# Kernel optimization log

Measured on AMD Instinct MI355X. Metric: run time of the kernel, lower is better.

The kernel has to match this reference:

```python
import jax, jax.numpy as jnp
import numpy as np

B, S, H = 4, 4096, 1024
NUM_LEVELS, DECAY = 3, 0.8
D0, D1 = 512, 204  # int(1024*0.5), int(512*0.5*0.8)


def _xavier(key, shape):
    fan_in, fan_out = shape
    return jax.random.normal(key, shape, dtype=jnp.float32) * np.sqrt(2.0 / (fan_in + fan_out))


def setup_inputs() -> dict:
    key = jax.random.key(0)
    ks = jax.random.split(key, 8)
    return {
        "keys": jax.random.normal(ks[0], (B, S, H), dtype=jnp.float32),
        "values": jax.random.normal(ks[1], (B, S, H), dtype=jnp.float32),
        "importance": jax.random.uniform(ks[2], (B, S), dtype=jnp.float32),
        # encoder layers (stored as [in, out]; torch Linear applies x @ W.T + b)
        "We0": _xavier(ks[3], (H, D0)), "be0": jnp.zeros((D0,), jnp.float32),
        "We1": _xavier(ks[4], (D0, D1)), "be1": jnp.zeros((D1,), jnp.float32),
        # decoder layers
        "Wd0": _xavier(ks[5], (D0, H)), "bd0": jnp.zeros((H,), jnp.float32),
        "Wd1": _xavier(ks[6], (D1, D0)), "bd1": jnp.zeros((D0,), jnp.float32),
    }


def _level_sizes(n):
    sizes, remaining = [], n
    for i in range(NUM_LEVELS):
        if i == NUM_LEVELS - 1:
            sizes.append(remaining)
        else:
            sz = int(remaining * (1 - DECAY) * DECAY ** i)
            sizes.append(sz)
            remaining -= sz
    return sizes


def reference(keys, values, importance, We0, be0, We1, be1, Wd0, bd0, Wd1, bd1):
    n = B * S
    fk = keys.reshape(n, H)
    fv = values.reshape(n, H)
    sorted_idx = jnp.argsort(-importance.reshape(-1))  # descending importance
    sizes = _level_sizes(n)

    def chain(x, level):
        # encode 0..level-1 with ReLU, then decode level-1..0 with ReLU
        if level >= 1:
            x = jax.nn.relu(x @ We0 + be0)
        if level >= 2:
            x = jax.nn.relu(x @ We1 + be1)
            x = jax.nn.relu(x @ Wd1 + bd1)
        if level >= 1:
            x = jax.nn.relu(x @ Wd0 + bd0)
        return x

    ck = jnp.zeros_like(fk)
    cv = jnp.zeros_like(fv)
    start = 0
    for level, size in enumerate(sizes):
        if size <= 0:
            continue
        idx = jax.lax.dynamic_slice(sorted_idx, (start,), (size,))
        ck = ck.at[idx].set(chain(fk[idx], level))
        cv = cv.at[idx].set(chain(fv[idx], level))
        start += size
    return ck.reshape(B, S, H), cv.reshape(B, S, H)
```

## Files before the change

### kernel.cpp

```cpp
#include <hip/hip_runtime.h>

typedef __attribute__((ext_vector_type(8))) short short8;
typedef __attribute__((ext_vector_type(4))) float f32x4;

#define N_TOK   16384
#define HDIM    1024
#define OUT_OFF 16777216
#define M1ROWS  26216
#define M2ROWS  22022
#define L2ROW0  4194

__device__ __forceinline__ unsigned short f2bf(float f) {
  unsigned int u = __float_as_uint(f);
  u += 0x7FFFu + ((u >> 16) & 1u);
  return (unsigned short)(u >> 16);
}

__device__ __forceinline__ void rowmap(int r, int& is_v, int& rank) {
  if (r < 2097)       { is_v = 0; rank = 3276 + r; }
  else if (r < 4194)  { is_v = 1; rank = 1179 + r; }
  else if (r < 15205) { is_v = 0; rank = 1179 + r; }
  else                { is_v = 1; rank = r - 9832; }
}

__global__ __launch_bounds__(256) void rank_count(const float* __restrict__ imp,
                                                  int* __restrict__ counts) {
  __shared__ float sj[2048];
  const int i = blockIdx.x * 256 + threadIdx.x;
  const int jbase = blockIdx.y * 2048;
  const float vi = imp[i];
  for (int s = threadIdx.x; s < 2048; s += 256) sj[s] = imp[jbase + s];
  __syncthreads();
  int cnt = 0;
  #pragma unroll 8
  for (int s = 0; s < 2048; ++s) {
    float vj = sj[s];
    bool gt = vj > vi;
    bool eq = (vj == vi) && ((jbase + s) < i);
    cnt += (gt || eq) ? 1 : 0;
  }
  atomicAdd(&counts[i], cnt);
}

__global__ __launch_bounds__(256) void scatter_order(const int* __restrict__ counts,
                                                     int* __restrict__ order) {
  int i = blockIdx.x * 256 + threadIdx.x;
  order[counts[i]] = i;
}

__global__ __launch_bounds__(256) void wconv(unsigned short* __restrict__ dst,
                                             const float* __restrict__ src,
                                             int Nd, int Kd, int Nsrc, int Ksrc) {
  int idx = blockIdx.x * 256 + threadIdx.x;
  if (idx >= Nd * Kd) return;
  int n = idx / Kd, k = idx % Kd;
  float v = (n < Nsrc && k < Ksrc) ? src[k * Nsrc + n] : 0.f;
  dst[idx] = f2bf(v);
}

__global__ __launch_bounds__(256) void gather_rows(unsigned short* __restrict__ X,
                                                   const float* __restrict__ keys,
                                                   const float* __restrict__ values,
                                                   const int* __restrict__ order) {
  int r = blockIdx.x;
  int is_v, rank; rowmap(r, is_v, rank);
  int token = order[rank];
  const float* src = (is_v ? values : keys) + (size_t)token * HDIM;
  int c = threadIdx.x * 4;
  float4 f = *reinterpret_cast<const float4*>(src + c);
  ushort4 h;
  h.x = f2bf(f.x); h.y = f2bf(f.y); h.z = f2bf(f.z); h.w = f2bf(f.w);
  *reinterpret_cast<ushort4*>(X + (size_t)r * HDIM + c) = h;
}

__global__ __launch_bounds__(256) void copy_level0(float* __restrict__ out,
                                                   const float* __restrict__ keys,
                                                   const float* __restrict__ values,
                                                   const int* __restrict__ order) {
  int b = blockIdx.x;
  int is_v = b & 1, rank = b >> 1;
  int token = order[rank];
  const float* src = (is_v ? values : keys) + (size_t)token * HDIM;
  float* dst = out + (is_v ? OUT_OFF : 0) + (size_t)token * HDIM;
  int c = threadIdx.x * 4;
  *reinterpret_cast<float4*>(dst + c) = *reinterpret_cast<const float4*>(src + c);
}

#define GLDS16(g, l) __builtin_amdgcn_global_load_lds( \
    (const __attribute__((address_space(1))) void*)(g), \
    (__attribute__((address_space(3))) void*)(l), 16, 0, 0)

template<int MODE, int K>
__global__ __launch_bounds__(512, 4) void g2(
    const unsigned short* __restrict__ A, int M,
    const unsigned short* __restrict__ Bt, int N,
    const float* __restrict__ bias, int Nbias,
    unsigned short* __restrict__ Cbf, int ldc,
    float* __restrict__ outf, const int* __restrict__ order,
    int NP, int NC) {
  constexpr int NH = K / 32;
  __shared__ __align__(16) unsigned short S[3][12288];

  const int bid = blockIdx.x;
  const int r8 = bid & 7, rest = bid >> 3;
  const int c8 = rest % NC, q8 = rest / NC;
  const int p8 = q8 * 8 + r8;
  if (p8 >= NP) return;
  const int row0 = p8 * 256, col0 = c8 * 128;

  const int tid = threadIdx.x;
  const int wave = tid >> 6, lane = tid & 63;
  const int wm = wave >> 1, wn = wave & 1;
  const int fr = lane & 15, lch = lane >> 4;

  const int lrow = lane >> 2;
  const int sswz = (((lane & 3) ^ ((lane >> 3) & 3)) << 3);
  const unsigned short* gp[3];
  int ldso[3];
  #pragma unroll
  for (int j = 0; j < 3; ++j) {
    const int g = wave * 3 + j;
    const bool isA = g < 16;
    int rr = isA ? (row0 + g * 16 + lrow) : (col0 + (g - 16) * 16 + lrow);
    const int lim = isA ? M : N;
    if (rr >= lim) rr = 0;
    gp[j] = (isA ? A : Bt) + (size_t)rr * K + sswz;
    ldso[j] = g * 512;
  }

  const int qoff = ((lch ^ ((fr >> 1) & 3)) << 3);
  const int abase = (wm * 64 + fr) * 32 + qoff;
  const int bbase = 8192 + (wn * 64 + fr) * 32 + qoff;

  f32x4 acc[4][4] = {};

  #pragma unroll
  for (int h = 0; h < 3; ++h)
    #pragma unroll
    for (int j = 0; j < 3; ++j)
      GLDS16(gp[j] + h * 32, S[h] + ldso[j]);
  asm volatile("s_waitcnt vmcnt(6)" ::: "memory");
  __builtin_amdgcn_s_barrier();

  int cur = 0;
  #pragma unroll 1
  for (int h = 0; h < NH; ++h) {
    const unsigned short* sl = S[cur];
    short8 a[4], b[4];
    #pragma unroll
    for (int m = 0; m < 4; ++m)
      a[m] = *reinterpret_cast<const short8*>(sl + abase + m * 512);
    #pragma unroll
    for (int n = 0; n < 4; ++n)
      b[n] = *reinterpret_cast<const short8*>(sl + bbase + n * 512);
    asm volatile("s_waitcnt lgkmcnt(0)" ::: "memory");
    __builtin_amdgcn_sched_barrier(0);
    __builtin_amdgcn_s_barrier();
    __builtin_amdgcn_s_setprio(1);
    #pragma unroll
    for (int m = 0; m < 4; ++m)
      #pragma unroll
      for (int n = 0; n < 4; ++n)
        acc[m][n] = __builtin_amdgcn_mfma_f32_16x16x32_bf16(a[m], b[n], acc[m][n], 0, 0, 0);
    __builtin_amdgcn_s_setprio(0);
    if (h + 3 < NH) {
      const int kc = (h + 3) * 32;
      #pragma unroll
      for (int j = 0; j < 3; ++j) GLDS16(gp[j] + kc, S[cur] + ldso[j]);
      asm volatile("s_waitcnt vmcnt(6)" ::: "memory");
    } else if (h + 2 < NH) {
      asm volatile("s_waitcnt vmcnt(3)" ::: "memory");
    } else if (h + 1 < NH) {
      asm volatile("s_waitcnt vmcnt(0)" ::: "memory");
    }
    __builtin_amdgcn_s_barrier();
    cur = (cur == 2) ? 0 : cur + 1;
  }

  const int orow = lch * 4;
  if (MODE == 0) {
    #pragma unroll
    for (int m = 0; m < 4; ++m) {
      #pragma unroll
      for (int n = 0; n < 4; ++n) {
        #pragma unroll
        for (int j = 0; j < 4; ++j) {
          int r = row0 + wm * 64 + m * 16 + orow + j;
          int c = col0 + wn * 64 + n * 16 + fr;
          if (r < M && c < N) {
            float v = acc[m][n][j] + (c < Nbias ? bias[c] : 0.f);
            Cbf[(size_t)r * ldc + c] = f2bf(fmaxf(v, 0.f));
          }
        }
      }
    }
  } else {
    float* Cl = (float*)S;
    #pragma unroll 1
    for (int p = 0; p < 4; ++p) {
      __builtin_amdgcn_s_barrier();
      if (wm == p) {
        #pragma unroll
        for (int m = 0; m < 4; ++m)
          #pragma unroll
          for (int n = 0; n < 4; ++n)
            #pragma unroll
            for (int j = 0; j < 4; ++j) {
              int rr = m * 16 + orow + j;
              int cc = wn * 64 + n * 16 + fr;
              float v = acc[m][n][j] + bias[col0 + cc];
              Cl[rr * 132 + cc] = fmaxf(v, 0.f);
            }
      }
      __builtin_amdgcn_s_barrier();
      #pragma unroll
      for (int u = 0; u < 4; ++u) {
        int unit = tid + u * 512;
        int rr = unit >> 5, ch = unit & 31;
        int r = row0 + p * 64 + rr;
        if (r < M) {
          int iv, rk; rowmap(r, iv, rk);
          int token = order[rk];
          f32x4 v = *reinterpret_cast<const f32x4*>(Cl + rr * 132 + ch * 4);
          *reinterpret_cast<f32x4*>(outf + (size_t)(iv ? OUT_OFF : 0) +
                                    (size_t)token * HDIM + col0 + ch * 4) = v;
        }
      }
    }
  }
}

static inline int swzg(int NP, int NC) { return 8 * NC * ((NP + 7) / 8); }

extern "C" void kernel_launch(void* const* d_in, const int* in_sizes, int n_in,
                              void* d_out, int out_size, void* d_ws, size_t ws_size,
                              hipStream_t stream) {
  const float* keys   = (const float*)d_in[0];
  const float* values = (const float*)d_in[1];
  const float* imp    = (const float*)d_in[2];
  const float* We0    = (const float*)d_in[3];
  const float* be0    = (const float*)d_in[4];
  const float* We1    = (const float*)d_in[5];
  const float* be1    = (const float*)d_in[6];
  const float* Wd0    = (const float*)d_in[7];
  const float* bd0    = (const float*)d_in[8];
  const float* Wd1    = (const float*)d_in[9];
  const float* bd1    = (const float*)d_in[10];

  char* ws = (char*)d_ws;
  int* counts           = (int*)(ws);
  int* order            = (int*)(ws + 65536);
  unsigned short* We0T  = (unsigned short*)(ws + 131072);
  unsigned short* We1T  = (unsigned short*)(ws + 1179648);
  unsigned short* Wd1T  = (unsigned short*)(ws + 1441792);
  unsigned short* Wd0T  = (unsigned short*)(ws + 1703936);
  unsigned short* Y     = (unsigned short*)(ws + 2752512);
  unsigned short* Z     = (unsigned short*)(ws + 29597696);
  unsigned short* X     = (unsigned short*)(ws + 40872960);
  float* outf = (float*)d_out;

  hipMemsetAsync(counts, 0, 65536, stream);
  rank_count<<<dim3(64, 8), 256, 0, stream>>>(imp, counts);
  scatter_order<<<64, 256, 0, stream>>>(counts, order);

  wconv<<<2048, 256, 0, stream>>>(We0T, We0, 512, 1024, 512, 1024);
  wconv<<<512,  256, 0, stream>>>(We1T, We1, 256, 512, 204, 512);
  wconv<<<512,  256, 0, stream>>>(Wd1T, Wd1, 512, 256, 512, 204);
  wconv<<<2048, 256, 0, stream>>>(Wd0T, Wd0, 1024, 512, 1024, 512);

  gather_rows<<<M1ROWS, 256, 0, stream>>>(X, keys, values, order);
  copy_level0<<<6552, 256, 0, stream>>>(outf, keys, values, order);

  g2<0, 1024><<<swzg(103, 4), 512, 0, stream>>>(
      X, M1ROWS, We0T, 512, be0, 512, Y, 512, nullptr, nullptr, 103, 4);

  g2<0, 512><<<swzg(87, 2), 512, 0, stream>>>(
      Y + (size_t)L2ROW0 * 512, M2ROWS, We1T, 256, be1, 204, Z, 256,
      nullptr, nullptr, 87, 2);

  g2<0, 256><<<swzg(87, 4), 512, 0, stream>>>(
      Z, M2ROWS, Wd1T, 512, bd1, 512, Y + (size_t)L2ROW0 * 512, 512,
      nullptr, nullptr, 87, 4);

  g2<1, 512><<<swzg(103, 8), 512, 0, stream>>>(
      Y, M1ROWS, Wd0T, 1024, bd0, 1024, nullptr, 0, outf, order, 103, 8);
}
```

Measured before the change: 276.6 us.

## Fuse row gather and bf16 conversion into first encoder GEMM; merge weight conversions

Removes the separate gather_rows kernel and the intermediate bf16 X buffer. The new first-layer GEMM kernel (128x128 tiles, 256 threads) reads fp32 keys/values rows through the sort order, converts them to bf16 in registers and stores them to LDS while prefetching the next chunk. The four weight-conversion launches are merged into one kernel. This saves a full write and re-read of the gathered activations plus launch overhead. In exchange the A operand no longer uses async global-to-LDS loads, the A reads are wider fp32 data, and the tile is smaller.

Measured after the change: 285.9 us. +3.3%, slower.

```diff
diff --git a/kernel.cpp b/kernel.cpp
--- a/kernel.cpp
+++ b/kernel.cpp
@@ -48,29 +48,20 @@
   order[counts[i]] = i;
 }
 
-__global__ __launch_bounds__(256) void wconv(unsigned short* __restrict__ dst,
-                                             const float* __restrict__ src,
-                                             int Nd, int Kd, int Nsrc, int Ksrc) {
-  int idx = blockIdx.x * 256 + threadIdx.x;
-  if (idx >= Nd * Kd) return;
+__global__ __launch_bounds__(256) void wconv4(
+    unsigned short* __restrict__ We0T, const float* __restrict__ We0,
+    unsigned short* __restrict__ We1T, const float* __restrict__ We1,
+    unsigned short* __restrict__ Wd1T, const float* __restrict__ Wd1,
+    unsigned short* __restrict__ Wd0T, const float* __restrict__ Wd0) {
+  int b = blockIdx.x;
+  unsigned short* dst; const float* src; int Kd, Nsrc, Ksrc, idx;
+  if (b < 2048)      { dst = We0T; src = We0; Kd = 1024; Nsrc = 512;  Ksrc = 1024; idx = b * 256 + threadIdx.x; }
+  else if (b < 2560) { dst = We1T; src = We1; Kd = 512;  Nsrc = 204;  Ksrc = 512;  idx = (b - 2048) * 256 + threadIdx.x; }
+  else if (b < 3072) { dst = Wd1T; src = Wd1; Kd = 256;  Nsrc = 512;  Ksrc = 204;  idx = (b - 2560) * 256 + threadIdx.x; }
+  else               { dst = Wd0T; src = Wd0; Kd = 512;  Nsrc = 1024; Ksrc = 512;  idx = (b - 3072) * 256 + threadIdx.x; }
   int n = idx / Kd, k = idx % Kd;
   float v = (n < Nsrc && k < Ksrc) ? src[k * Nsrc + n] : 0.f;
   dst[idx] = f2bf(v);
-}
-
-__global__ __launch_bounds__(256) void gather_rows(unsigned short* __restrict__ X,
-                                                   const float* __restrict__ keys,
-                                                   const float* __restrict__ values,
-                                                   const int* __restrict__ order) {
-  int r = blockIdx.x;
-  int is_v, rank; rowmap(r, is_v, rank);
-  int token = order[rank];
-  const float* src = (is_v ? values : keys) + (size_t)token * HDIM;
-  int c = threadIdx.x * 4;
-  float4 f = *reinterpret_cast<const float4*>(src + c);
-  ushort4 h;
-  h.x = f2bf(f.x); h.y = f2bf(f.y); h.z = f2bf(f.z); h.w = f2bf(f.w);
-  *reinterpret_cast<ushort4*>(X + (size_t)r * HDIM + c) = h;
 }
 
 __global__ __launch_bounds__(256) void copy_level0(float* __restrict__ out,
@@ -90,6 +81,151 @@
     (const __attribute__((address_space(1))) void*)(g), \
     (__attribute__((address_space(3))) void*)(l), 16, 0, 0)
 
+template<int K>
+__global__ __launch_bounds__(256, 3) void g1f(
+    const float* __restrict__ keys, const float* __restrict__ values,
+    const int* __restrict__ order, int M,
+    const unsigned short* __restrict__ Bt, int N,
+    const float* __restrict__ bias,
+    unsigned short* __restrict__ Y, int ldc, int NP, int NC) {
+  constexpr int NH = K / 32;
+  __shared__ __align__(16) unsigned short S[3][8192];
+
+  const int bid = blockIdx.x;
+  const int r8 = bid & 7, rest = bid >> 3;
+  const int c8 = rest % NC, q8 = rest / NC;
+  const int p8 = q8 * 8 + r8;
+  if (p8 >= NP) return;
+  const int row0 = p8 * 128, col0 = c8 * 128;
+
+  const int tid = threadIdx.x;
+  const int wave = tid >> 6, lane = tid & 63;
+  const int wm = wave >> 1, wn = wave & 1;
+  const int fr = lane & 15, lch = lane >> 4;
+
+  const int rin = lane >> 2;
+  const int qc = lane & 3;
+  const int xr = (lane >> 3) & 3;
+  const int pchunk = qc ^ xr;
+
+  const float* asrc[2]; int awoff[2];
+  #pragma unroll
+  for (int j = 0; j < 2; ++j) {
+    int s = wave * 2 + j;
+    int gr = row0 + s * 16 + rin; if (gr >= M) gr = 0;
+    int iv, rk; rowmap(gr, iv, rk);
+    int token = order[rk];
+    asrc[j] = (iv ? values : keys) + (size_t)token * HDIM + qc * 8;
+    awoff[j] = (s * 16 + rin) * 32 + pchunk * 8;
+  }
+  const unsigned short* bsrc[2]; int bldso[2];
+  #pragma unroll
+  for (int j = 0; j < 2; ++j) {
+    int s = wave * 2 + j;
+    int cr = col0 + s * 16 + rin; if (cr >= N) cr = 0;
+    bsrc[j] = Bt + (size_t)cr * K + pchunk * 8;
+    bldso[j] = 4096 + s * 512;
+  }
+
+  const int qoff = ((lch ^ ((fr >> 1) & 3)) << 3);
+  const int abase = (wm * 64 + fr) * 32 + qoff;
+  const int bbase = 4096 + (wn * 64 + fr) * 32 + qoff;
+
+  f32x4 acc[4][4] = {};
+  float4 pa[2][2];
+
+  #pragma unroll
+  for (int hp = 0; hp < 3; ++hp) {
+    #pragma unroll
+    for (int j = 0; j < 2; ++j) {
+      float4 lo = *reinterpret_cast<const float4*>(asrc[j] + hp * 32);
+      float4 hi = *reinterpret_cast<const float4*>(asrc[j] + hp * 32 + 4);
+      uint4 wv;
+      wv.x = (unsigned)f2bf(lo.x) | ((unsigned)f2bf(lo.y) << 16);
+      wv.y = (unsigned)f2bf(lo.z) | ((unsigned)f2bf(lo.w) << 16);
+      wv.z = (unsigned)f2bf(hi.x) | ((unsigned)f2bf(hi.y) << 16);
+      wv.w = (unsigned)f2bf(hi.z) | ((unsigned)f2bf(hi.w) << 16);
+      *reinterpret_cast<uint4*>(&S[hp][awoff[j]]) = wv;
+    }
+  }
+  #pragma unroll
+  for (int hp = 0; hp < 3; ++hp)
+    #pragma unroll
+    for (int j = 0; j < 2; ++j)
+      GLDS16(bsrc[j] + hp * 32, (unsigned short*)S[hp] + bldso[j]);
+  asm volatile("s_waitcnt vmcnt(0)" ::: "memory");
+  #pragma unroll
+  for (int j = 0; j < 2; ++j) {
+    pa[j][0] = *reinterpret_cast<const float4*>(asrc[j] + 3 * 32);
+    pa[j][1] = *reinterpret_cast<const float4*>(asrc[j] + 3 * 32 + 4);
+  }
+  asm volatile("s_waitcnt lgkmcnt(0)" ::: "memory");
+  __builtin_amdgcn_s_barrier();
+
+  int sh = 0;
+  #pragma unroll 1
+  for (int h = 0; h < NH; ++h) {
+    const unsigned short* sl = S[sh];
+    short8 a[4], b[4];
+    #pragma unroll
+    for (int m = 0; m < 4; ++m)
+      a[m] = *reinterpret_cast<const short8*>(sl + abase + m * 512);
+    #pragma unroll
+    for (int n = 0; n < 4; ++n)
+      b[n] = *reinterpret_cast<const short8*>(sl + bbase + n * 512);
+    asm volatile("s_waitcnt lgkmcnt(0)" ::: "memory");
+    __builtin_amdgcn_sched_barrier(0);
+    if (h + 3 < NH) asm volatile("s_waitcnt vmcnt(6)" ::: "memory");
+    else            asm volatile("s_waitcnt vmcnt(0)" ::: "memory");
+    __builtin_amdgcn_sched_barrier(0);
+    __builtin_amdgcn_s_barrier();
+    __builtin_amdgcn_s_setprio(1);
+    #pragma unroll
+    for (int m = 0; m < 4; ++m)
+      #pragma unroll
+      for (int n = 0; n < 4; ++n)
+        acc[m][n] = __builtin_amdgcn_mfma_f32_16x16x32_bf16(a[m], b[n], acc[m][n], 0, 0, 0);
+    __builtin_amdgcn_s_setprio(0);
+    if (h + 3 < NH) {
+      #pragma unroll
+      for (int j = 0; j < 2; ++j) {
+        uint4 wv;
+        wv.x = (unsigned)f2bf(pa[j][0].x) | ((unsigned)f2bf(pa[j][0].y) << 16);
+        wv.y = (unsigned)f2bf(pa[j][0].z) | ((unsigned)f2bf(pa[j][0].w) << 16);
+        wv.z = (unsigned)f2bf(pa[j][1].x) | ((unsigned)f2bf(pa[j][1].y) << 16);
+        wv.w = (unsigned)f2bf(pa[j][1].z) | ((unsigned)f2bf(pa[j][1].w) << 16);
+        *reinterpret_cast<uint4*>(&S[sh][awoff[j]]) = wv;
+      }
+      if (h + 4 < NH) {
+        #pragma unroll
+        for (int j = 0; j < 2; ++j) {
+          pa[j][0] = *reinterpret_cast<const float4*>(asrc[j] + (h + 4) * 32);
+          pa[j][1] = *reinterpret_cast<const float4*>(asrc[j] + (h + 4) * 32 + 4);
+        }
+      }
+      #pragma unroll
+      for (int j = 0; j < 2; ++j)
+        GLDS16(bsrc[j] + (h + 3) * 32, (unsigned short*)S[sh] + bldso[j]);
+    }
+    sh = (sh == 2) ? 0 : sh + 1;
+  }
+
+  const int orow = lch * 4;
+  #pragma unroll
+  for (int m = 0; m < 4; ++m)
+    #pragma unroll
+    for (int n = 0; n < 4; ++n)
+      #pragma unroll
+      for (int j = 0; j < 4; ++j) {
+        int r = row0 + wm * 64 + m * 16 + orow + j;
+        int c = col0 + wn * 64 + n * 16 + fr;
+        if (r < M) {
+          float v = acc[m][n][j] + bias[c];
+          Y[(size_t)r * ldc + c] = f2bf(fmaxf(v, 0.f));
+        }
+      }
+}
+
 template<int MODE, int K>
 __global__ __launch_bounds__(512, 4) void g2(
     const unsigned short* __restrict__ A, int M,
@@ -180,9 +316,9 @@
   const int orow = lch * 4;
   if (MODE == 0) {
     #pragma unroll
-    for (int m = 0; m < 4; ++m) {
-      #pragma unroll
-      for (int n = 0; n < 4; ++n) {
+    for (int m = 0; m < 4; ++m)
+      #pragma unroll
+      for (int n = 0; n < 4; ++n)
         #pragma unroll
         for (int j = 0; j < 4; ++j) {
           int r = row0 + wm * 64 + m * 16 + orow + j;
@@ -192,8 +328,6 @@
             Cbf[(size_t)r * ldc + c] = f2bf(fmaxf(v, 0.f));
           }
         }
-      }
-    }
   } else {
     float* Cl = (float*)S;
     #pragma unroll 1
@@ -256,23 +390,17 @@
   unsigned short* Wd0T  = (unsigned short*)(ws + 1703936);
   unsigned short* Y     = (unsigned short*)(ws + 2752512);
   unsigned short* Z     = (unsigned short*)(ws + 29597696);
-  unsigned short* X     = (unsigned short*)(ws + 40872960);
   float* outf = (float*)d_out;
 
   hipMemsetAsync(counts, 0, 65536, stream);
   rank_count<<<dim3(64, 8), 256, 0, stream>>>(imp, counts);
   scatter_order<<<64, 256, 0, stream>>>(counts, order);
 
-  wconv<<<2048, 256, 0, stream>>>(We0T, We0, 512, 1024, 512, 1024);
-  wconv<<<512,  256, 0, stream>>>(We1T, We1, 256, 512, 204, 512);
-  wconv<<<512,  256, 0, stream>>>(Wd1T, Wd1, 512, 256, 512, 204);
-  wconv<<<2048, 256, 0, stream>>>(Wd0T, Wd0, 1024, 512, 1024, 512);
-
-  gather_rows<<<M1ROWS, 256, 0, stream>>>(X, keys, values, order);
+  wconv4<<<5120, 256, 0, stream>>>(We0T, We0, We1T, We1, Wd1T, Wd1, Wd0T, Wd0);
   copy_level0<<<6552, 256, 0, stream>>>(outf, keys, values, order);
 
-  g2<0, 1024><<<swzg(103, 4), 512, 0, stream>>>(
-      X, M1ROWS, We0T, 512, be0, 512, Y, 512, nullptr, nullptr, 103, 4);
+  g1f<1024><<<swzg(205, 4), 256, 0, stream>>>(
+      keys, values, order, M1ROWS, We0T, 512, be0, Y, 512, 205, 4);
 
   g2<0, 512><<<swzg(87, 2), 512, 0, stream>>>(
       Y + (size_t)L2ROW0 * 512, M2ROWS, We1T, 256, be1, 204, Z, 256,
```

## Shrink GEMM tiles to 128x128 with 4 waves and fuse prep kernels

Applied to the files above, without the earlier changes.

Merges the four weight conversions, the row gather and the level-0 copy into one launch, removing per-launch overhead and letting those memory-bound pieces run concurrently. The GEMM kernel moves from 256x128 tiles with 8 waves to 128x128 tiles with 4 waves, which gives more blocks for the small-M problems. Its pipeline becomes a prefetch-distance-2 scheme over three LDS buffers with the barrier at the top of each step, and the setprio hints are dropped. Smaller tiles lower the data reuse per block and double the number of blocks.

Result: no change. 271.3 us (-1.9%).

```diff
diff --git a/kernel.cpp b/kernel.cpp
--- a/kernel.cpp
+++ b/kernel.cpp
@@ -48,42 +48,43 @@
   order[counts[i]] = i;
 }
 
-__global__ __launch_bounds__(256) void wconv(unsigned short* __restrict__ dst,
-                                             const float* __restrict__ src,
-                                             int Nd, int Kd, int Nsrc, int Ksrc) {
-  int idx = blockIdx.x * 256 + threadIdx.x;
-  if (idx >= Nd * Kd) return;
-  int n = idx / Kd, k = idx % Kd;
-  float v = (n < Nsrc && k < Ksrc) ? src[k * Nsrc + n] : 0.f;
-  dst[idx] = f2bf(v);
-}
-
-__global__ __launch_bounds__(256) void gather_rows(unsigned short* __restrict__ X,
-                                                   const float* __restrict__ keys,
-                                                   const float* __restrict__ values,
-                                                   const int* __restrict__ order) {
-  int r = blockIdx.x;
-  int is_v, rank; rowmap(r, is_v, rank);
-  int token = order[rank];
-  const float* src = (is_v ? values : keys) + (size_t)token * HDIM;
-  int c = threadIdx.x * 4;
-  float4 f = *reinterpret_cast<const float4*>(src + c);
-  ushort4 h;
-  h.x = f2bf(f.x); h.y = f2bf(f.y); h.z = f2bf(f.z); h.w = f2bf(f.w);
-  *reinterpret_cast<ushort4*>(X + (size_t)r * HDIM + c) = h;
-}
-
-__global__ __launch_bounds__(256) void copy_level0(float* __restrict__ out,
-                                                   const float* __restrict__ keys,
-                                                   const float* __restrict__ values,
-                                                   const int* __restrict__ order) {
+__global__ __launch_bounds__(256) void prep_fused(
+    unsigned short* __restrict__ We0T, const float* __restrict__ We0,
+    unsigned short* __restrict__ We1T, const float* __restrict__ We1,
+    unsigned short* __restrict__ Wd1T, const float* __restrict__ Wd1,
+    unsigned short* __restrict__ Wd0T, const float* __restrict__ Wd0,
+    unsigned short* __restrict__ X,
+    const float* __restrict__ keys, const float* __restrict__ values,
+    const int* __restrict__ order, float* __restrict__ out) {
   int b = blockIdx.x;
-  int is_v = b & 1, rank = b >> 1;
-  int token = order[rank];
-  const float* src = (is_v ? values : keys) + (size_t)token * HDIM;
-  float* dst = out + (is_v ? OUT_OFF : 0) + (size_t)token * HDIM;
-  int c = threadIdx.x * 4;
-  *reinterpret_cast<float4*>(dst + c) = *reinterpret_cast<const float4*>(src + c);
+  if (b < 5120) {
+    unsigned short* dst; const float* src; int Kd, Nsrc, Ksrc, idx;
+    if (b < 2048)      { dst = We0T; src = We0; Kd = 1024; Nsrc = 512;  Ksrc = 1024; idx = b * 256 + threadIdx.x; }
+    else if (b < 2560) { dst = We1T; src = We1; Kd = 512;  Nsrc = 204;  Ksrc = 512;  idx = (b - 2048) * 256 + threadIdx.x; }
+    else if (b < 3072) { dst = Wd1T; src = Wd1; Kd = 256;  Nsrc = 512;  Ksrc = 204;  idx = (b - 2560) * 256 + threadIdx.x; }
+    else               { dst = Wd0T; src = Wd0; Kd = 512;  Nsrc = 1024; Ksrc = 512;  idx = (b - 3072) * 256 + threadIdx.x; }
+    int n = idx / Kd, k = idx % Kd;
+    float v = (n < Nsrc && k < Ksrc) ? src[k * Nsrc + n] : 0.f;
+    dst[idx] = f2bf(v);
+  } else if (b < 5120 + M1ROWS) {
+    int r = b - 5120;
+    int is_v, rank; rowmap(r, is_v, rank);
+    int token = order[rank];
+    const float* src = (is_v ? values : keys) + (size_t)token * HDIM;
+    int c = threadIdx.x * 4;
+    float4 f = *reinterpret_cast<const float4*>(src + c);
+    ushort4 h;
+    h.x = f2bf(f.x); h.y = f2bf(f.y); h.z = f2bf(f.z); h.w = f2bf(f.w);
+    *reinterpret_cast<ushort4*>(X + (size_t)r * HDIM + c) = h;
+  } else {
+    int bb = b - (5120 + M1ROWS);
+    int is_v = bb & 1, rank = bb >> 1;
+    int token = order[rank];
+    const float* src = (is_v ? values : keys) + (size_t)token * HDIM;
+    float* dst = out + (is_v ? OUT_OFF : 0) + (size_t)token * HDIM;
+    int c = threadIdx.x * 4;
+    *reinterpret_cast<float4*>(dst + c) = *reinterpret_cast<const float4*>(src + c);
+  }
 }
 
 #define GLDS16(g, l) __builtin_amdgcn_global_load_lds( \
@@ -91,7 +92,7 @@
     (__attribute__((address_space(3))) void*)(l), 16, 0, 0)
 
 template<int MODE, int K>
-__global__ __launch_bounds__(512, 4) void g2(
+__global__ __launch_bounds__(256, 4) void g128(
     const unsigned short* __restrict__ A, int M,
     const unsigned short* __restrict__ Bt, int N,
     const float* __restrict__ bias, int Nbias,
@@ -99,14 +100,14 @@
     float* __restrict__ outf, const int* __restrict__ order,
     int NP, int NC) {
   constexpr int NH = K / 32;
-  __shared__ __align__(16) unsigned short S[3][12288];
+  __shared__ __align__(16) unsigned short S[3][8192];
 
   const int bid = blockIdx.x;
   const int r8 = bid & 7, rest = bid >> 3;
   const int c8 = rest % NC, q8 = rest / NC;
   const int p8 = q8 * 8 + r8;
   if (p8 >= NP) return;
-  const int row0 = p8 * 256, col0 = c8 * 128;
+  const int row0 = p8 * 128, col0 = c8 * 128;
 
   const int tid = threadIdx.x;
   const int wave = tid >> 6, lane = tid & 63;
@@ -115,13 +116,13 @@
 
   const int lrow = lane >> 2;
   const int sswz = (((lane & 3) ^ ((lane >> 3) & 3)) << 3);
-  const unsigned short* gp[3];
-  int ldso[3];
+  const unsigned short* gp[4];
+  int ldso[4];
   #pragma unroll
-  for (int j = 0; j < 3; ++j) {
-    const int g = wave * 3 + j;
-    const bool isA = g < 16;
-    int rr = isA ? (row0 + g * 16 + lrow) : (col0 + (g - 16) * 16 + lrow);
+  for (int j = 0; j < 4; ++j) {
+    const int g = wave * 4 + j;
+    const bool isA = g < 8;
+    int rr = isA ? (row0 + g * 16 + lrow) : (col0 + (g - 8) * 16 + lrow);
     const int lim = isA ? M : N;
     if (rr >= lim) rr = 0;
     gp[j] = (isA ? A : Bt) + (size_t)rr * K + sswz;
@@ -130,21 +131,22 @@
 
   const int qoff = ((lch ^ ((fr >> 1) & 3)) << 3);
   const int abase = (wm * 64 + fr) * 32 + qoff;
-  const int bbase = 8192 + (wn * 64 + fr) * 32 + qoff;
+  const int bbase = 4096 + (wn * 64 + fr) * 32 + qoff;
 
   f32x4 acc[4][4] = {};
 
   #pragma unroll
-  for (int h = 0; h < 3; ++h)
-    #pragma unroll
-    for (int j = 0; j < 3; ++j)
-      GLDS16(gp[j] + h * 32, S[h] + ldso[j]);
-  asm volatile("s_waitcnt vmcnt(6)" ::: "memory");
-  __builtin_amdgcn_s_barrier();
+  for (int j = 0; j < 4; ++j) GLDS16(gp[j], S[0] + ldso[j]);
+  #pragma unroll
+  for (int j = 0; j < 4; ++j) GLDS16(gp[j] + 32, S[1] + ldso[j]);
 
   int cur = 0;
   #pragma unroll 1
-  for (int h = 0; h < NH; ++h) {
+  for (int t = 0; t < NH; ++t) {
+    if (t + 1 < NH) asm volatile("s_waitcnt vmcnt(4)" ::: "memory");
+    else            asm volatile("s_waitcnt vmcnt(0)" ::: "memory");
+    __builtin_amdgcn_s_barrier();
+    __builtin_amdgcn_sched_barrier(0);
     const unsigned short* sl = S[cur];
     short8 a[4], b[4];
     #pragma unroll
@@ -153,36 +155,26 @@
     #pragma unroll
     for (int n = 0; n < 4; ++n)
       b[n] = *reinterpret_cast<const short8*>(sl + bbase + n * 512);
-    asm volatile("s_waitcnt lgkmcnt(0)" ::: "memory");
-    __builtin_amdgcn_sched_barrier(0);
-    __builtin_amdgcn_s_barrier();
-    __builtin_amdgcn_s_setprio(1);
+    if (t + 2 < NH) {
+      const int kc = (t + 2) * 32;
+      int nb = cur + 2; if (nb >= 3) nb -= 3;
+      #pragma unroll
+      for (int j = 0; j < 4; ++j) GLDS16(gp[j] + kc, S[nb] + ldso[j]);
+    }
     #pragma unroll
     for (int m = 0; m < 4; ++m)
       #pragma unroll
       for (int n = 0; n < 4; ++n)
         acc[m][n] = __builtin_amdgcn_mfma_f32_16x16x32_bf16(a[m], b[n], acc[m][n], 0, 0, 0);
-    __builtin_amdgcn_s_setprio(0);
-    if (h + 3 < NH) {
-      const int kc = (h + 3) * 32;
-      #pragma unroll
-      for (int j = 0; j < 3; ++j) GLDS16(gp[j] + kc, S[cur] + ldso[j]);
-      asm volatile("s_waitcnt vmcnt(6)" ::: "memory");
-    } else if (h + 2 < NH) {
-      asm volatile("s_waitcnt vmcnt(3)" ::: "memory");
-    } else if (h + 1 < NH) {
-      asm volatile("s_waitcnt vmcnt(0)" ::: "memory");
-    }
-    __builtin_amdgcn_s_barrier();
     cur = (cur == 2) ? 0 : cur + 1;
   }
 
   const int orow = lch * 4;
   if (MODE == 0) {
     #pragma unroll
-    for (int m = 0; m < 4; ++m) {
-      #pragma unroll
-      for (int n = 0; n < 4; ++n) {
+    for (int m = 0; m < 4; ++m)
+      #pragma unroll
+      for (int n = 0; n < 4; ++n)
         #pragma unroll
         for (int j = 0; j < 4; ++j) {
           int r = row0 + wm * 64 + m * 16 + orow + j;
@@ -192,12 +184,10 @@
             Cbf[(size_t)r * ldc + c] = f2bf(fmaxf(v, 0.f));
           }
         }
-      }
-    }
   } else {
     float* Cl = (float*)S;
     #pragma unroll 1
-    for (int p = 0; p < 4; ++p) {
+    for (int p = 0; p < 2; ++p) {
       __builtin_amdgcn_s_barrier();
       if (wm == p) {
         #pragma unroll
@@ -214,8 +204,8 @@
       }
       __builtin_amdgcn_s_barrier();
       #pragma unroll
-      for (int u = 0; u < 4; ++u) {
-        int unit = tid + u * 512;
+      for (int u = 0; u < 8; ++u) {
+        int unit = tid + u * 256;
         int rr = unit >> 5, ch = unit & 31;
         int r = row0 + p * 64 + rr;
         if (r < M) {
@@ -263,25 +253,20 @@
   rank_count<<<dim3(64, 8), 256, 0, stream>>>(imp, counts);
   scatter_order<<<64, 256, 0, stream>>>(counts, order);
 
-  wconv<<<2048, 256, 0, stream>>>(We0T, We0, 512, 1024, 512, 1024);
-  wconv<<<512,  256, 0, stream>>>(We1T, We1, 256, 512, 204, 512);
-  wconv<<<512,  256, 0, stream>>>(Wd1T, Wd1, 512, 256, 512, 204);
-  wconv<<<2048, 256, 0, stream>>>(Wd0T, Wd0, 1024, 512, 1024, 512);
-
-  gather_rows<<<M1ROWS, 256, 0, stream>>>(X, keys, values, order);
-  copy_level0<<<6552, 256, 0, stream>>>(outf, keys, values, order);
-
-  g2<0, 1024><<<swzg(103, 4), 512, 0, stream>>>(
-      X, M1ROWS, We0T, 512, be0, 512, Y, 512, nullptr, nullptr, 103, 4);
-
-  g2<0, 512><<<swzg(87, 2), 512, 0, stream>>>(
+  prep_fused<<<5120 + M1ROWS + 6552, 256, 0, stream>>>(
+      We0T, We0, We1T, We1, Wd1T, Wd1, Wd0T, Wd0, X, keys, values, order, outf);
+
+  g128<0, 1024><<<swzg(205, 4), 256, 0, stream>>>(
+      X, M1ROWS, We0T, 512, be0, 512, Y, 512, nullptr, nullptr, 205, 4);
+
+  g128<0, 512><<<swzg(173, 2), 256, 0, stream>>>(
       Y + (size_t)L2ROW0 * 512, M2ROWS, We1T, 256, be1, 204, Z, 256,
-      nullptr, nullptr, 87, 2);
-
-  g2<0, 256><<<swzg(87, 4), 512, 0, stream>>>(
+      nullptr, nullptr, 173, 2);
+
+  g128<0, 256><<<swzg(173, 4), 256, 0, stream>>>(
       Z, M2ROWS, Wd1T, 512, bd1, 512, Y + (size_t)L2ROW0 * 512, 512,
-      nullptr, nullptr, 87, 4);
-
-  g2<1, 512><<<swzg(103, 8), 512, 0, stream>>>(
-      Y, M1ROWS, Wd0T, 1024, bd0, 1024, nullptr, 0, outf, order, 103, 8);
-}
+      nullptr, nullptr, 173, 4);
+
+  g128<1, 512><<<swzg(205, 8), 256, 0, stream>>>(
+      Y, M1ROWS, Wd0T, 1024, bd0, 1024, nullptr, 0, outf, order, 205, 8);
+}
```
